# Kernel tuning notes

Measured on AMD Instinct MI355X. Metric: run time of the kernel, lower is better.

## Reference

```python
import jax, jax.numpy as jnp
import numpy as np
import math

B, S, H, NH = 1, 2048, 1024, 16  # batch, seq, hidden, heads


def setup_inputs() -> dict:
    key = jax.random.key(0)
    ks = jax.random.split(key, 12)
    inp = {
        "query": jax.random.normal(ks[0], (B, S, H), dtype=jnp.float32),
        "key": jax.random.normal(ks[1], (B, S, H), dtype=jnp.float32),
        "value": jax.random.normal(ks[2], (B, S, H), dtype=jnp.float32),
        "attention_mask": jax.random.randint(ks[3], (1, 1, S, S), 0, 2, dtype=jnp.int32),
        # torch nn.Linear params: y = x @ W.T + b, W init ~ U(-1/sqrt(H), 1/sqrt(H))
        "Wq": jax.random.uniform(ks[4], (H, H), jnp.float32, -1, 1) / math.sqrt(H),
        "bq": jax.random.uniform(ks[5], (H,), jnp.float32, -1, 1) / math.sqrt(H),
        "Wk": jax.random.uniform(ks[6], (H, H), jnp.float32, -1, 1) / math.sqrt(H),
        "bk": jax.random.uniform(ks[7], (H,), jnp.float32, -1, 1) / math.sqrt(H),
        "Wv": jax.random.uniform(ks[8], (H, H), jnp.float32, -1, 1) / math.sqrt(H),
        "bv": jax.random.uniform(ks[9], (H,), jnp.float32, -1, 1) / math.sqrt(H),
        "Wo": jax.random.uniform(ks[10], (H, H), jnp.float32, -1, 1) / math.sqrt(H),
        "bo": jax.random.uniform(ks[11], (H,), jnp.float32, -1, 1) / math.sqrt(H),
        "head": NH,
        "hidden_size": H,
    }
    return inp


def reference(query, key, value, attention_mask, Wq, bq, Wk, bk, Wv, bv, Wo, bo, head, hidden_size):
    b, s, _ = query.shape
    d_k = hidden_size // head

    def proj(x, W, bias):
        # [b, s, hidden] -> [b, head, s, d_k]
        y = x @ W.T + bias
        return y.reshape(b, s, head, d_k).transpose(0, 2, 1, 3)

    q = proj(query, Wq, bq)
    k = proj(key, Wk, bk)
    v = proj(value, Wv, bv)

    # naive full score matrix, as in the source (scale by sqrt(d_k) = last dim of q)
    scores = jnp.einsum("bhqd,bhkd->bhqk", q, k) / math.sqrt(d_k)
    # faithful quirk: masked positions are set to 0 (not -inf) before softmax
    scores = jnp.where(attention_mask == 0, jnp.zeros((), scores.dtype), scores)
    attn = jax.nn.softmax(scores, axis=-1)

    out = jnp.einsum("bhqk,bhkd->bhqd", attn, v)  # [b, head, s, d_k]
    out = out.transpose(0, 2, 1, 3).reshape(b, s, head * d_k)
    return out @ Wo.T + bo
```

## Files before the change

### kernel.cpp

```cpp
#include <hip/hip_runtime.h>
#include <hip/hip_bf16.h>


#define S_LEN 2048
#define HID   1024
#define NHEAD 16
#define DK    64

typedef unsigned short u16;
typedef __attribute__((ext_vector_type(8))) short bf16x8;
typedef __attribute__((ext_vector_type(4))) float f32x4;

#if defined(__has_builtin)
#if __has_builtin(__builtin_amdgcn_exp2f)
#define EXP2F(x) __builtin_amdgcn_exp2f(x)
#else
#define EXP2F(x) exp2f(x)
#endif
#else
#define EXP2F(x) exp2f(x)
#endif

__device__ __forceinline__ void load16_lds(const void* g, void* l) {
  __builtin_amdgcn_global_load_lds(
      (const __attribute__((address_space(1))) void*)g,
      (__attribute__((address_space(3))) void*)l, 16, 0, 0);
}

__device__ __forceinline__ short bfbits(float x) {
  __hip_bfloat16 h = __float2bfloat16(x);
  return *(short*)&h;
}
__device__ __forceinline__ bf16x8 cvt8(float4 a, float4 b) {
  bf16x8 r;
  r[0] = bfbits(a.x); r[1] = bfbits(a.y); r[2] = bfbits(a.z); r[3] = bfbits(a.w);
  r[4] = bfbits(b.x); r[5] = bfbits(b.y); r[6] = bfbits(b.z); r[7] = bfbits(b.w);
  return r;
}
__device__ __forceinline__ float bf2f(u16 u) {
  unsigned v = (unsigned)u << 16;
  return *(float*)&v;
}

__global__ __launch_bounds__(256) void prep_kernel(
    const float* __restrict__ wq, const float* __restrict__ wk,
    const float* __restrict__ wv, const float* __restrict__ wo,
    const int* __restrict__ mask, u16* __restrict__ Wbf,
    unsigned int* __restrict__ bits) {
  const int y = blockIdx.y;
  if (y < 4) {
    const float* src = y == 0 ? wq : (y == 1 ? wk : (y == 2 ? wv : wo));
    size_t i = ((size_t)blockIdx.x * 256 + threadIdx.x) * 8;
    float4 a = *(const float4*)(src + i);
    float4 b = *(const float4*)(src + i + 4);
    *(bf16x8*)(Wbf + (size_t)y * (HID * HID) + i) = cvt8(a, b);
  } else {
    int w = blockIdx.x * 256 + threadIdx.x;
    const int4* p = (const int4*)(mask + (size_t)w * 32);
    unsigned word = 0;
#pragma unroll
    for (int i = 0; i < 8; ++i) {
      int4 v = p[i];
      word |= (unsigned)(v.x != 0) << (i * 4 + 0);
      word |= (unsigned)(v.y != 0) << (i * 4 + 1);
      word |= (unsigned)(v.z != 0) << (i * 4 + 2);
      word |= (unsigned)(v.w != 0) << (i * 4 + 3);
    }
    bits[w] = word;
  }
}

__global__ __launch_bounds__(256) void gemm_qkv(
    const float* __restrict__ qf32, const float* __restrict__ kf32,
    const float* __restrict__ vf32, const u16* __restrict__ Wbf,
    const float* __restrict__ bq, const float* __restrict__ bk,
    const float* __restrict__ bv, u16* __restrict__ Qb,
    u16* __restrict__ Kb, u16* __restrict__ Vt) {
  constexpr int Mm = 2048, Nn = 1024, Kk = 1024, NIT = 16;
  const int z = blockIdx.z;
  const float* A = z == 0 ? qf32 : (z == 1 ? kf32 : vf32);
  const u16* W = Wbf + (size_t)z * (HID * HID);
  const float* bias = z == 0 ? bq : (z == 1 ? bk : bv);
  u16* C = z == 0 ? Qb : (z == 1 ? Kb : Vt);
  const float oscale = (z == 0) ? 0.125f * 1.4426950408889634f : 1.0f;
  const int transpose = (z == 2);

  const int tid = threadIdx.x, lane = tid & 63, wave = tid >> 6;
  const int q4 = lane >> 4, c16 = lane & 15;
  const int bx = blockIdx.x;
  const int mBase = (bx & 31) * 64;
  const int nBase = (bx >> 5) * 128;
  const int wn = wave * 32;

  __shared__ __align__(16) u16 As[2][2][64 * 32];
  __shared__ __align__(16) u16 Bs[2][2][128 * 32];

  f32x4 acc[4][2] = {};
  const int srow = lane >> 2, se8 = (lane & 3) * 8;

  auto issueW = [&](int it, int buf) {
#pragma unroll
    for (int j = 0; j < 4; ++j) {
      int u = wave * 4 + j, h = u >> 3, grp = u & 7;
      load16_lds(W + (size_t)(nBase + grp * 16 + srow) * Kk + it * 64 +
                     h * 32 + se8,
                 &Bs[buf][h][grp * 512]);
    }
  };
  float4 ar[2][2];
  auto loadA = [&](int it) {
#pragma unroll
    for (int j = 0; j < 2; ++j) {
      int u = wave * 2 + j, h = u >> 2, grp = u & 3;
      const float* s = A + (size_t)(mBase + grp * 16 + srow) * Kk + it * 64 +
                       h * 32 + se8;
      ar[j][0] = *(const float4*)s;
      ar[j][1] = *(const float4*)(s + 4);
    }
  };
  auto storeA = [&](int buf) {
#pragma unroll
    for (int j = 0; j < 2; ++j) {
      int u = wave * 2 + j, h = u >> 2, grp = u & 3;
      *(bf16x8*)&As[buf][h][grp * 512 + srow * 32 + se8] =
          cvt8(ar[j][0], ar[j][1]);
    }
  };

  loadA(0);
  storeA(0);
  issueW(0, 0);
  __syncthreads();

  for (int it = 0; it < NIT; ++it) {
    const int buf = it & 1, nbuf = buf ^ 1;
    if (it + 1 < NIT) {
      issueW(it + 1, nbuf);
      loadA(it + 1);
    }
#pragma unroll
    for (int kk = 0; kk < 2; ++kk) {
      bf16x8 af[4], bfr[2];
#pragma unroll
      for (int t = 0; t < 4; ++t)
        af[t] = *(const bf16x8*)&As[buf][kk][(t * 16 + c16) * 32 + q4 * 8];
#pragma unroll
      for (int t = 0; t < 2; ++t)
        bfr[t] = *(const bf16x8*)&Bs[buf][kk][(wn + t * 16 + c16) * 32 + q4 * 8];
#pragma unroll
      for (int mt = 0; mt < 4; ++mt)
#pragma unroll
        for (int nt = 0; nt < 2; ++nt)
          acc[mt][nt] = __builtin_amdgcn_mfma_f32_16x16x32_bf16(
              af[mt], bfr[nt], acc[mt][nt], 0, 0, 0);
    }
    if (it + 1 < NIT) storeA(nbuf);
    __syncthreads();
  }

#pragma unroll
  for (int nt = 0; nt < 2; ++nt) {
    int col = nBase + wn + nt * 16 + c16;
    float bv2 = bias[col];
#pragma unroll
    for (int mt = 0; mt < 4; ++mt) {
#pragma unroll
      for (int r = 0; r < 4; ++r) {
        int row = mBase + mt * 16 + q4 * 4 + r;
        float v = (acc[mt][nt][r] + bv2) * oscale;
        if (transpose)
          ((__hip_bfloat16*)C)[(size_t)col * Mm + row] = __float2bfloat16(v);
        else
          ((__hip_bfloat16*)C)[(size_t)row * Nn + col] = __float2bfloat16(v);
      }
    }
  }
}

__global__ __launch_bounds__(256) void attn_kernel(
    const u16* __restrict__ Qb, const u16* __restrict__ Kb,
    const u16* __restrict__ Vt, const unsigned* __restrict__ mbits,
    u16* __restrict__ partO, float* __restrict__ partL) {
  const int qt = blockIdx.x, h = blockIdx.y, zz = blockIdx.z;
  const int nita = (S_LEN / 64) / gridDim.z;
  const int tid = threadIdx.x, lane = tid & 63, wave = tid >> 6;
  const int q4 = lane >> 4, c16 = lane & 15;

  __shared__ __align__(16) u16 Ks[2][2][64 * 32];
  __shared__ __align__(16) u16 Vs[2][2][64 * 32];
  __shared__ __align__(16) u16 Ps[4][2 * 16 * 72];

  const int wq0 = qt * 128 + wave * 32;

  bf16x8 qf[2][2];
#pragma unroll
  for (int t = 0; t < 2; ++t)
#pragma unroll
    for (int kk = 0; kk < 2; ++kk)
      qf[t][kk] = *(const bf16x8*)(Qb + (size_t)(wq0 + t * 16 + c16) * HID +
                                   h * DK + kk * 32 + q4 * 8);

  f32x4 o[2][4] = {};
  float l_lane[2][4] = {};

  const int srow = lane >> 2;
  const int se8  = (lane & 3) * 8;
  const int kvbase = zz * nita * 64;

  auto issueKV = [&](int it, int buf) {
    const int kv0 = kvbase + it * 64;
#pragma unroll
    for (int j = 0; j < 4; ++j) {
      int i = wave * 4 + j;
      if (i < 8) {
        int half = i >> 2, grp = i & 3;
        load16_lds(Kb + (size_t)(kv0 + grp * 16 + srow) * HID + h * DK +
                       half * 32 + se8,
                   &Ks[buf][half][grp * 512]);
      } else {
        int ii = i - 8;
        int half = ii >> 2, grp = ii & 3;
        load16_lds(Vt + (size_t)(h * DK + grp * 16 + srow) * S_LEN + kv0 +
                       half * 32 + se8,
                   &Vs[buf][half][grp * 512]);
      }
    }
  };

  issueKV(0, 0);
  __syncthreads();

  for (int it = 0; it < nita; ++it) {
    const int buf = it & 1, nbuf = buf ^ 1;
    const int kv0 = kvbase + it * 64;
    if (it + 1 < nita) issueKV(it + 1, nbuf);

    f32x4 sv[2][4];
#pragma unroll
    for (int nt = 0; nt < 4; ++nt) {
      bf16x8 kf0 = *(const bf16x8*)&Ks[buf][0][(nt * 16 + c16) * 32 + q4 * 8];
      bf16x8 kf1 = *(const bf16x8*)&Ks[buf][1][(nt * 16 + c16) * 32 + q4 * 8];
#pragma unroll
      for (int t = 0; t < 2; ++t) {
        f32x4 a = {};
        a = __builtin_amdgcn_mfma_f32_16x16x32_bf16(qf[t][0], kf0, a, 0, 0, 0);
        a = __builtin_amdgcn_mfma_f32_16x16x32_bf16(qf[t][1], kf1, a, 0, 0, 0);
        sv[t][nt] = a;
      }
    }

#pragma unroll
    for (int t = 0; t < 2; ++t)
#pragma unroll
      for (int r = 0; r < 4; ++r) {
        int row = wq0 + t * 16 + q4 * 4 + r;
        const unsigned* mrow = mbits + (size_t)row * 64 + (kv0 >> 5);
        unsigned w0 = mrow[0], w1 = mrow[1];
#pragma unroll
        for (int nt = 0; nt < 4; ++nt) {
          unsigned word = (nt < 2) ? w0 : w1;
          int bit = ((nt & 1) * 16) + c16;
          float s = ((word >> bit) & 1u) ? sv[t][nt][r] : 0.0f;
          float p = EXP2F(s);
          sv[t][nt][r] = p;
          l_lane[t][r] += p;
        }
      }

    u16* pw = &Ps[wave][0];
#pragma unroll
    for (int t = 0; t < 2; ++t)
#pragma unroll
      for (int r = 0; r < 4; ++r)
#pragma unroll
        for (int nt = 0; nt < 4; ++nt)
          ((__hip_bfloat16*)pw)[t * 1152 + (q4 * 4 + r) * 72 + nt * 16 + c16] =
              __float2bfloat16(sv[t][nt][r]);
    asm volatile("s_waitcnt lgkmcnt(0)" ::: "memory");

    bf16x8 vb[2][4];
#pragma unroll
    for (int kk = 0; kk < 2; ++kk)
#pragma unroll
      for (int nt = 0; nt < 4; ++nt)
        vb[kk][nt] =
            *(const bf16x8*)&Vs[buf][kk][(nt * 16 + c16) * 32 + q4 * 8];
#pragma unroll
    for (int t = 0; t < 2; ++t)
#pragma unroll
      for (int kk = 0; kk < 2; ++kk) {
        bf16x8 pa = *(const bf16x8*)&pw[t * 1152 + c16 * 72 + kk * 32 + q4 * 8];
#pragma unroll
        for (int nt = 0; nt < 4; ++nt)
          o[t][nt] = __builtin_amdgcn_mfma_f32_16x16x32_bf16(pa, vb[kk][nt],
                                                             o[t][nt], 0, 0, 0);
      }
    __syncthreads();
  }

#pragma unroll
  for (int t = 0; t < 2; ++t)
#pragma unroll
    for (int r = 0; r < 4; ++r) {
      float s = l_lane[t][r];
#pragma unroll
      for (int d = 1; d < 16; d <<= 1) s += __shfl_xor(s, d);
      l_lane[t][r] = s;
    }

#pragma unroll
  for (int t = 0; t < 2; ++t)
#pragma unroll
    for (int r = 0; r < 4; ++r) {
      int row = wq0 + t * 16 + q4 * 4 + r;
#pragma unroll
      for (int nt = 0; nt < 4; ++nt)
        ((__hip_bfloat16*)partO)[((size_t)zz * S_LEN + row) * HID + h * DK +
                                 nt * 16 + c16] = __float2bfloat16(o[t][nt][r]);
      if (c16 == 0)
        partL[((size_t)zz * NHEAD + h) * S_LEN + row] = l_lane[t][r];
    }
}

template <int NSPLIT>
__global__ __launch_bounds__(256) void gemm_out(
    const u16* __restrict__ partO, const float* __restrict__ partL,
    const u16* __restrict__ Wo, const float* __restrict__ bo,
    float* __restrict__ out) {
  constexpr int Nn = 1024, Kk = 1024, NIT = 16;
  constexpr size_t M2 = (size_t)S_LEN * HID;
  const int tid = threadIdx.x, lane = tid & 63, wave = tid >> 6;
  const int q4 = lane >> 4, c16 = lane & 15;
  const int bx = blockIdx.x;
  const int mBase = (bx & 63) * 32;
  const int nBase = (bx >> 6) * 128;
  const int wn = wave * 32;

  __shared__ __align__(16) u16 As[2][2][32 * 32];
  __shared__ __align__(16) u16 Bs[2][2][128 * 32];

  f32x4 acc[2][2] = {};
  const int srow = lane >> 2, se8 = (lane & 3) * 8;

  auto issueW = [&](int it, int buf) {
#pragma unroll
    for (int j = 0; j < 4; ++j) {
      int u = wave * 4 + j, h = u >> 3, grp = u & 7;
      load16_lds(Wo + (size_t)(nBase + grp * 16 + srow) * Kk + it * 64 +
                     h * 32 + se8,
                 &Bs[buf][h][grp * 512]);
    }
  };
  bf16x8 asr[NSPLIT];
  float invr;
  auto loadA = [&](int it) {
    int u = wave, h = u >> 1, grp = u & 1;
    int row = mBase + grp * 16 + srow;
    size_t off = (size_t)row * Kk + it * 64 + h * 32 + se8;
    float l = 0.f;
#pragma unroll
    for (int s = 0; s < NSPLIT; ++s) {
      asr[s] = *(const bf16x8*)(partO + (size_t)s * M2 + off);
      l += partL[((size_t)s * NHEAD + it) * S_LEN + row];
    }
    invr = 1.0f / l;
  };
  auto storeA = [&](int buf) {
    int u = wave, h = u >> 1, grp = u & 1;
    bf16x8 r;
#pragma unroll
    for (int j = 0; j < 8; ++j) {
      float v = bf2f((u16)asr[0][j]);
#pragma unroll
      for (int s = 1; s < NSPLIT; ++s) v += bf2f((u16)asr[s][j]);
      r[j] = bfbits(v * invr);
    }
    *(bf16x8*)&As[buf][h][grp * 512 + srow * 32 + se8] = r;
  };

  loadA(0);
  storeA(0);
  issueW(0, 0);
  __syncthreads();

  for (int it = 0; it < NIT; ++it) {
    const int buf = it & 1, nbuf = buf ^ 1;
    if (it + 1 < NIT) {
      issueW(it + 1, nbuf);
      loadA(it + 1);
    }
#pragma unroll
    for (int kk = 0; kk < 2; ++kk) {
      bf16x8 af[2], bfr[2];
#pragma unroll
      for (int t = 0; t < 2; ++t)
        af[t] = *(const bf16x8*)&As[buf][kk][(t * 16 + c16) * 32 + q4 * 8];
#pragma unroll
      for (int t = 0; t < 2; ++t)
        bfr[t] = *(const bf16x8*)&Bs[buf][kk][(wn + t * 16 + c16) * 32 + q4 * 8];
#pragma unroll
      for (int mt = 0; mt < 2; ++mt)
#pragma unroll
        for (int nt = 0; nt < 2; ++nt)
          acc[mt][nt] = __builtin_amdgcn_mfma_f32_16x16x32_bf16(
              af[mt], bfr[nt], acc[mt][nt], 0, 0, 0);
    }
    if (it + 1 < NIT) storeA(nbuf);
    __syncthreads();
  }

#pragma unroll
  for (int nt = 0; nt < 2; ++nt) {
    int col = nBase + wn + nt * 16 + c16;
    float bv = bo[col];
#pragma unroll
    for (int mt = 0; mt < 2; ++mt)
#pragma unroll
      for (int r = 0; r < 4; ++r) {
        int row = mBase + mt * 16 + q4 * 4 + r;
        out[(size_t)row * Nn + col] = acc[mt][nt][r] + bv;
      }
  }
}

extern "C" void kernel_launch(void* const* d_in, const int* in_sizes, int n_in,
                              void* d_out, int out_size, void* d_ws, size_t ws_size,
                              hipStream_t stream) {
  const float* q    = (const float*)d_in[0];
  const float* k    = (const float*)d_in[1];
  const float* v    = (const float*)d_in[2];
  const int*   mask = (const int*)d_in[3];
  const float* Wq = (const float*)d_in[4];
  const float* bq = (const float*)d_in[5];
  const float* Wk = (const float*)d_in[6];
  const float* bk = (const float*)d_in[7];
  const float* Wv = (const float*)d_in[8];
  const float* bv = (const float*)d_in[9];
  const float* Wo = (const float*)d_in[10];
  const float* bo = (const float*)d_in[11];

  const size_t M2 = (size_t)S_LEN * HID;
  const size_t W1 = (size_t)HID * HID;

  auto need_for = [&](int ns) {
    return (4 * W1 + (size_t)ns * M2 + 3 * M2) * 2 +
           (size_t)S_LEN * 64 * 4 + (size_t)ns * NHEAD * S_LEN * 4;
  };
  int nsplit = (ws_size >= need_for(4)) ? 4 : 2;
  if (ws_size < need_for(2)) return;

  u16* Wbf = (u16*)d_ws;
  u16* partO = Wbf + 4 * W1;
  u16* Qb = partO + (size_t)nsplit * M2;
  u16* Kb = Qb + M2;
  u16* Vt = Kb + M2;
  unsigned* mbits = (unsigned*)(Vt + M2);
  float* partL = (float*)(mbits + (size_t)S_LEN * 64);

  hipLaunchKernelGGL(prep_kernel, dim3(512, 5), dim3(256), 0, stream,
                     Wq, Wk, Wv, Wo, mask, Wbf, mbits);

  hipLaunchKernelGGL(gemm_qkv, dim3(256, 1, 3), dim3(256), 0, stream,
                     q, k, v, Wbf, bq, bk, bv, Qb, Kb, Vt);

  hipLaunchKernelGGL(attn_kernel, dim3(S_LEN / 128, NHEAD, nsplit), dim3(256),
                     0, stream, Qb, Kb, Vt, mbits, partO, partL);

  if (nsplit == 4)
    hipLaunchKernelGGL((gemm_out<4>), dim3(512), dim3(256), 0, stream,
                       partO, partL, Wbf + 3 * W1, bo, (float*)d_out);
  else
    hipLaunchKernelGGL((gemm_out<2>), dim3(512), dim3(256), 0, stream,
                       partO, partL, Wbf + 3 * W1, bo, (float*)d_out);
}
```

Baseline: 207.7 us.

## Halve GEMM tile widths to double block counts and fix attention split at two

The QKV projection GEMM changes from 64x128 to 64x64 tiles with a 2x2 wave layout, doubling its grid to 512x3 blocks. The output GEMM changes from 32x128 to 32x64 tiles with one 16-column MFMA strip per wave, doubling its grid to 1024 blocks. The attention key split is now always 2 instead of 4 when workspace allows, which halves the partial-output traffic and the reduction work in the output GEMM. The aim is more blocks per CU for better occupancy and latency hiding. In exchange there is less reuse per tile (A is reloaded twice as often), and the attention kernel has fewer blocks.

```diff
diff --git a/kernel.cpp b/kernel.cpp
--- a/kernel.cpp
+++ b/kernel.cpp
@@ -89,19 +89,19 @@
   const int q4 = lane >> 4, c16 = lane & 15;
   const int bx = blockIdx.x;
   const int mBase = (bx & 31) * 64;
-  const int nBase = (bx >> 5) * 128;
-  const int wn = wave * 32;
+  const int nBase = (bx >> 5) * 64;
+  const int wm = (wave >> 1) * 32, wn = (wave & 1) * 32;
 
   __shared__ __align__(16) u16 As[2][2][64 * 32];
-  __shared__ __align__(16) u16 Bs[2][2][128 * 32];
-
-  f32x4 acc[4][2] = {};
+  __shared__ __align__(16) u16 Bs[2][2][64 * 32];
+
+  f32x4 acc[2][2] = {};
   const int srow = lane >> 2, se8 = (lane & 3) * 8;
 
   auto issueW = [&](int it, int buf) {
 #pragma unroll
-    for (int j = 0; j < 4; ++j) {
-      int u = wave * 4 + j, h = u >> 3, grp = u & 7;
+    for (int j = 0; j < 2; ++j) {
+      int u = wave * 2 + j, h = u >> 2, grp = u & 3;
       load16_lds(W + (size_t)(nBase + grp * 16 + srow) * Kk + it * 64 +
                      h * 32 + se8,
                  &Bs[buf][h][grp * 512]);
@@ -140,15 +140,15 @@
     }
 #pragma unroll
     for (int kk = 0; kk < 2; ++kk) {
-      bf16x8 af[4], bfr[2];
-#pragma unroll
-      for (int t = 0; t < 4; ++t)
-        af[t] = *(const bf16x8*)&As[buf][kk][(t * 16 + c16) * 32 + q4 * 8];
+      bf16x8 af[2], bfr[2];
+#pragma unroll
+      for (int t = 0; t < 2; ++t)
+        af[t] = *(const bf16x8*)&As[buf][kk][(wm + t * 16 + c16) * 32 + q4 * 8];
 #pragma unroll
       for (int t = 0; t < 2; ++t)
         bfr[t] = *(const bf16x8*)&Bs[buf][kk][(wn + t * 16 + c16) * 32 + q4 * 8];
 #pragma unroll
-      for (int mt = 0; mt < 4; ++mt)
+      for (int mt = 0; mt < 2; ++mt)
 #pragma unroll
         for (int nt = 0; nt < 2; ++nt)
           acc[mt][nt] = __builtin_amdgcn_mfma_f32_16x16x32_bf16(
@@ -163,10 +163,10 @@
     int col = nBase + wn + nt * 16 + c16;
     float bv2 = bias[col];
 #pragma unroll
-    for (int mt = 0; mt < 4; ++mt) {
+    for (int mt = 0; mt < 2; ++mt) {
 #pragma unroll
       for (int r = 0; r < 4; ++r) {
-        int row = mBase + mt * 16 + q4 * 4 + r;
+        int row = mBase + wm + mt * 16 + q4 * 4 + r;
         float v = (acc[mt][nt][r] + bv2) * oscale;
         if (transpose)
           ((__hip_bfloat16*)C)[(size_t)col * Mm + row] = __float2bfloat16(v);
@@ -333,19 +333,19 @@
   const int q4 = lane >> 4, c16 = lane & 15;
   const int bx = blockIdx.x;
   const int mBase = (bx & 63) * 32;
-  const int nBase = (bx >> 6) * 128;
-  const int wn = wave * 32;
+  const int nBase = (bx >> 6) * 64;
+  const int wn = wave * 16;
 
   __shared__ __align__(16) u16 As[2][2][32 * 32];
-  __shared__ __align__(16) u16 Bs[2][2][128 * 32];
-
-  f32x4 acc[2][2] = {};
+  __shared__ __align__(16) u16 Bs[2][2][64 * 32];
+
+  f32x4 acc[2] = {};
   const int srow = lane >> 2, se8 = (lane & 3) * 8;
 
   auto issueW = [&](int it, int buf) {
 #pragma unroll
-    for (int j = 0; j < 4; ++j) {
-      int u = wave * 4 + j, h = u >> 3, grp = u & 7;
+    for (int j = 0; j < 2; ++j) {
+      int u = wave * 2 + j, h = u >> 2, grp = u & 3;
       load16_lds(Wo + (size_t)(nBase + grp * 16 + srow) * Kk + it * 64 +
                      h * 32 + se8,
                  &Bs[buf][h][grp * 512]);
@@ -391,34 +391,29 @@
     }
 #pragma unroll
     for (int kk = 0; kk < 2; ++kk) {
-      bf16x8 af[2], bfr[2];
+      bf16x8 af[2], bfr;
 #pragma unroll
       for (int t = 0; t < 2; ++t)
         af[t] = *(const bf16x8*)&As[buf][kk][(t * 16 + c16) * 32 + q4 * 8];
-#pragma unroll
-      for (int t = 0; t < 2; ++t)
-        bfr[t] = *(const bf16x8*)&Bs[buf][kk][(wn + t * 16 + c16) * 32 + q4 * 8];
+      bfr = *(const bf16x8*)&Bs[buf][kk][(wn + c16) * 32 + q4 * 8];
 #pragma unroll
       for (int mt = 0; mt < 2; ++mt)
-#pragma unroll
-        for (int nt = 0; nt < 2; ++nt)
-          acc[mt][nt] = __builtin_amdgcn_mfma_f32_16x16x32_bf16(
-              af[mt], bfr[nt], acc[mt][nt], 0, 0, 0);
+        acc[mt] = __builtin_amdgcn_mfma_f32_16x16x32_bf16(
+            af[mt], bfr, acc[mt], 0, 0, 0);
     }
     if (it + 1 < NIT) storeA(nbuf);
     __syncthreads();
   }
 
-#pragma unroll
-  for (int nt = 0; nt < 2; ++nt) {
-    int col = nBase + wn + nt * 16 + c16;
+  {
+    int col = nBase + wn + c16;
     float bv = bo[col];
 #pragma unroll
     for (int mt = 0; mt < 2; ++mt)
 #pragma unroll
       for (int r = 0; r < 4; ++r) {
         int row = mBase + mt * 16 + q4 * 4 + r;
-        out[(size_t)row * Nn + col] = acc[mt][nt][r] + bv;
+        out[(size_t)row * Nn + col] = acc[mt][r] + bv;
       }
   }
 }
@@ -446,8 +441,8 @@
     return (4 * W1 + (size_t)ns * M2 + 3 * M2) * 2 +
            (size_t)S_LEN * 64 * 4 + (size_t)ns * NHEAD * S_LEN * 4;
   };
-  int nsplit = (ws_size >= need_for(4)) ? 4 : 2;
-  if (ws_size < need_for(2)) return;
+  int nsplit = (ws_size >= need_for(2)) ? 2 : 0;
+  if (!nsplit) return;
 
   u16* Wbf = (u16*)d_ws;
   u16* partO = Wbf + 4 * W1;
@@ -460,16 +455,12 @@
   hipLaunchKernelGGL(prep_kernel, dim3(512, 5), dim3(256), 0, stream,
                      Wq, Wk, Wv, Wo, mask, Wbf, mbits);
 
-  hipLaunchKernelGGL(gemm_qkv, dim3(256, 1, 3), dim3(256), 0, stream,
+  hipLaunchKernelGGL(gemm_qkv, dim3(512, 1, 3), dim3(256), 0, stream,
                      q, k, v, Wbf, bq, bk, bv, Qb, Kb, Vt);
 
   hipLaunchKernelGGL(attn_kernel, dim3(S_LEN / 128, NHEAD, nsplit), dim3(256),
                      0, stream, Qb, Kb, Vt, mbits, partO, partL);
 
-  if (nsplit == 4)
-    hipLaunchKernelGGL((gemm_out<4>), dim3(512), dim3(256), 0, stream,
-                       partO, partL, Wbf + 3 * W1, bo, (float*)d_out);
-  else
-    hipLaunchKernelGGL((gemm_out<2>), dim3(512), dim3(256), 0, stream,
-                       partO, partL, Wbf + 3 * W1, bo, (float*)d_out);
-}
+  hipLaunchKernelGGL((gemm_out<2>), dim3(1024), dim3(256), 0, stream,
+                     partO, partL, Wbf + 3 * W1, bo, (float*)d_out);
+}
```

Result: slower. 223.9 us (+7.8%).
